# Optimization experiments

Hardware: AMD Instinct MI355X
Metric: run time of the kernel (lower is better)

Reference implementation:

```python
import jax, jax.numpy as jnp
import numpy as np

I = 2048  # input_size
O = 2048  # output_size
K = 16    # number of parallel linears

def setup_inputs() -> dict:
    key = jax.random.key(0)
    ks = jax.random.split(key, 8)
    s_in = 1.0 / np.sqrt(I)
    s_cat = 1.0 / np.sqrt(K * O)
    x = jax.random.normal(ks[0], (4, 2048, I), dtype=jnp.float32)
    W16 = jax.random.uniform(ks[1], (K, O, I), jnp.float32, -s_in, s_in)   # stacked weights of 16 Linears
    b16 = jax.random.uniform(ks[2], (K, O), jnp.float32, -s_in, s_in)
    Wf = jax.random.uniform(ks[3], (O, K * O), jnp.float32, -s_cat, s_cat)  # fusion Linear weight
    bf = jax.random.uniform(ks[4], (O,), jnp.float32, -s_cat, s_cat)
    gamma = jnp.ones((O,), jnp.float32)  # LayerNorm weight
    beta = jnp.zeros((O,), jnp.float32)  # LayerNorm bias
    return {"x": x, "W16": W16, "b16": b16, "Wf": Wf, "bf": bf, "gamma": gamma, "beta": beta}

def reference(x, W16, b16, Wf, bf, gamma, beta):
    B, S, _ = x.shape
    # 16 parallel Linears as one batched GEMM; k index order == torch.cat order
    y = jnp.einsum('bsi,koi->bsko', x, W16) + b16          # [B,S,16,O]
    combined = y.reshape(B, S, K * O)                       # concat along last dim
    fused = jnp.einsum('bsc,oc->bso', combined, Wf) + bf    # fusion linear [B,S,O]
    # LayerNorm (eps=1e-5, torch default)
    mu = jnp.mean(fused, axis=-1, keepdims=True)
    var = jnp.mean(jnp.square(fused - mu), axis=-1, keepdims=True)
    normed = (fused - mu) * jax.lax.rsqrt(var + 1e-5) * gamma + beta
    # exact (erf) GELU matching torch nn.GELU default; dropout(p=0.005) is identity at eval
    return jax.nn.gelu(normed, approximate=False)
```

## Files before the change

### kernel.cpp

```cpp
#include <hip/hip_runtime.h>
#include <hip/hip_bf16.h>
#include <math.h>


typedef __bf16 bf16_t;
typedef __bf16 bf16x8 __attribute__((ext_vector_type(8)));
typedef __bf16 bf16x4 __attribute__((ext_vector_type(4)));
typedef float  f32x4  __attribute__((ext_vector_type(4)));

#define KC 32768
#define OD 2048
#define ID 2048
#define BSROWS 8192

#define GLL16(g, l) __builtin_amdgcn_global_load_lds( \
    (const __attribute__((address_space(1))) void*)(g), \
    (__attribute__((address_space(3))) void*)(l), 16, 0, 0)

__device__ __forceinline__ float wave_sum(float v) {
#pragma unroll
  for (int o = 32; o > 0; o >>= 1) v += __shfl_down(v, o, 64);
  return v;
}

__global__ __launch_bounds__(512, 1) void gemm256(
    const bf16_t* __restrict__ A, const bf16_t* __restrict__ B,
    float* __restrict__ C, int M, int N, int lda, int ldb,
    int Ks, int nbn, int mn)
{
  __shared__ char lds[131072];
  const int tid  = threadIdx.x;
  const int lane = tid & 63;
  const int wave = tid >> 6;

  const int nwg = gridDim.x;
  const int per = nwg >> 3;
  const int swz = (blockIdx.x & 7) * per + (blockIdx.x >> 3);
  const int z   = swz / mn;
  const int rem = swz - z * mn;
  const int bm  = (rem / nbn) * 256;
  const int bn  = (rem % nbn) * 256;
  const int k0  = z * Ks;
  float* Cz = C + (size_t)z * ((size_t)M * (size_t)N);

  const int wr = wave >> 2, wc = wave & 3;
  const int frow  = lane & 15;
  const int bhalf = wc >> 1;

  const int rdsl0 = (((lane >> 4))     ^ (lane & 7)) * 16;
  const int rdsl1 = (((lane >> 4) + 4) ^ (lane & 7)) * 16;

  const int abase = wr * 16384 + frow * 128;
  const int bloc  = ((wc & 1) * 64 + frow) * 128;

  const int srow8 = tid >> 3;
  const int sw8   = (tid & 7) ^ (srow8 & 7);
  const bf16_t* gA0 = A + (size_t)(bm + srow8) * lda + k0 + sw8 * 8;
  const bf16_t* gB0 = B + (size_t)(bn + srow8) * ldb + k0 + sw8 * 8;
  const int ldw = wave * 1024;

  f32x4 acc[8][4] = {};
  bf16x8 aqE[2][2], aqO[2][2], bA[4][2], bB[4][2];
  const int NT = Ks >> 6;

#define STAGE_A_HALF(t, hf) do {                                          \
    _Pragma("unroll") for (int s_ = 0; s_ < 2; ++s_)                      \
      GLL16(gA0 + (size_t)((hf) * 128 + s_ * 64) * lda + (size_t)(t) * 64,\
            lds + (((t) & 1) << 15) + (hf) * 16384 + s_ * 8192 + ldw);    \
  } while (0)

#define STAGE_B_HALF(t, hh) do {                                          \
    _Pragma("unroll") for (int s_ = 0; s_ < 2; ++s_)                      \
      GLL16(gB0 + (size_t)((hh) * 128 + s_ * 64) * ldb + (size_t)(t) * 64,\
            lds + 65536 + ((((t) * 2 + (hh)) & 3) << 14) + s_ * 8192 + ldw); \
  } while (0)

#define READ_AQ(t, q, aq) do {                                            \
    const char* p_ = lds + (((t) & 1) << 15) + abase + (q) * 4096;        \
    aq[0][0] = *reinterpret_cast<const bf16x8*>(p_ + rdsl0);              \
    aq[0][1] = *reinterpret_cast<const bf16x8*>(p_ + rdsl1);              \
    aq[1][0] = *reinterpret_cast<const bf16x8*>(p_ + 2048 + rdsl0);       \
    aq[1][1] = *reinterpret_cast<const bf16x8*>(p_ + 2048 + rdsl1);       \
  } while (0)

#define READ_BH(t, kh, bg) do {                                           \
    const char* p_ = lds + 65536 + ((((t) * 2 + bhalf) & 3) << 14) + bloc;\
    _Pragma("unroll") for (int n_ = 0; n_ < 4; ++n_)                      \
      bg[n_][kh] = *reinterpret_cast<const bf16x8*>(                      \
          p_ + n_ * 2048 + ((kh) ? rdsl1 : rdsl0));                       \
  } while (0)

#define SYNCPH() do {                                                     \
    __builtin_amdgcn_s_barrier();                                         \
    asm volatile("s_waitcnt lgkmcnt(0)" ::: "memory");                    \
    __builtin_amdgcn_sched_barrier(0);                                    \
  } while (0)

#define MFMA_Q(q, aq, bg) do {                                            \
    __builtin_amdgcn_s_setprio(1);                                        \
    _Pragma("unroll") for (int mh_ = 0; mh_ < 2; ++mh_)                   \
      _Pragma("unroll") for (int n_ = 0; n_ < 4; ++n_) {                  \
        acc[2*(q)+mh_][n_] = __builtin_amdgcn_mfma_f32_16x16x32_bf16(     \
            aq[mh_][0], bg[n_][0], acc[2*(q)+mh_][n_], 0, 0, 0);          \
        acc[2*(q)+mh_][n_] = __builtin_amdgcn_mfma_f32_16x16x32_bf16(     \
            aq[mh_][1], bg[n_][1], acc[2*(q)+mh_][n_], 0, 0, 0);          \
      }                                                                   \
    __builtin_amdgcn_s_setprio(0);                                        \
  } while (0)

#define TILE(t, BC, BN) do {                                              \
                                                                  \
    if ((t) + 1 < NT) STAGE_A_HALF((t) + 1, 0);                           \
    READ_AQ((t), 0, aqE);                                                 \
    SYNCPH(); MFMA_Q(0, aqE, BC);                                         \
                                                                  \
    if ((t) + 1 < NT) STAGE_A_HALF((t) + 1, 1);                           \
    READ_AQ((t), 1, aqO);                                                 \
    SYNCPH(); MFMA_Q(1, aqO, BC);                                         \
    if ((t) + 1 < NT) {                \
      asm volatile("s_waitcnt vmcnt(4)" ::: "memory");                    \
      __builtin_amdgcn_s_barrier();                                       \
    }                                                                     \
                                                                  \
    if ((t) + 2 < NT) STAGE_B_HALF((t) + 2, 0);                           \
    READ_AQ((t), 2, aqE);                                                 \
    if ((t) + 1 < NT) READ_BH((t) + 1, 0, BN);                            \
    SYNCPH(); MFMA_Q(2, aqE, BC);                                         \
                                                                  \
    if ((t) + 2 < NT) STAGE_B_HALF((t) + 2, 1);                           \
    READ_AQ((t), 3, aqO);                                                 \
    if ((t) + 1 < NT) READ_BH((t) + 1, 1, BN);                            \
    SYNCPH(); MFMA_Q(3, aqO, BC);                                         \
    if ((t) + 2 < NT) {                \
      asm volatile("s_waitcnt vmcnt(4)" ::: "memory");                    \
      __builtin_amdgcn_s_barrier();                                       \
    } else if ((t) + 1 < NT) {                                            \
      asm volatile("s_waitcnt vmcnt(0)" ::: "memory");    \
      __builtin_amdgcn_s_barrier();                                       \
    }                                                                     \
  } while (0)

  STAGE_A_HALF(0, 0); STAGE_A_HALF(0, 1);
  STAGE_B_HALF(0, 0); STAGE_B_HALF(0, 1);
  STAGE_B_HALF(1, 0); STAGE_B_HALF(1, 1);
  asm volatile("s_waitcnt vmcnt(4)" ::: "memory");
  __builtin_amdgcn_s_barrier();
  READ_BH(0, 0, bA);
  READ_BH(0, 1, bA);
  asm volatile("s_waitcnt lgkmcnt(0)" ::: "memory");
  __builtin_amdgcn_sched_barrier(0);
  __builtin_amdgcn_s_barrier();

#pragma unroll 1
  for (int t = 0; t < NT; t += 2) {
    TILE(t,     bA, bB);
    TILE(t + 1, bB, bA);
  }
#undef TILE
#undef MFMA_Q
#undef SYNCPH
#undef READ_BH
#undef READ_AQ
#undef STAGE_B_HALF
#undef STAGE_A_HALF

  const int wrbase = wr * 128, wcbase = wc * 64;
  const int cr = (lane >> 4) * 4, cc = lane & 15;
#pragma unroll
  for (int m = 0; m < 8; ++m)
#pragma unroll
    for (int n = 0; n < 4; ++n) {
      size_t base = (size_t)(bm + wrbase + m * 16 + cr) * N + (bn + wcbase + n * 16 + cc);
#pragma unroll
      for (int j = 0; j < 4; ++j)
        Cz[base + (size_t)j * N] = acc[m][n][j];
    }
}

__global__ void conv_wf_beq(const float* __restrict__ Wf, const float* __restrict__ b16,
                            bf16_t* __restrict__ Wf16, float* __restrict__ beq)
{
  const int o  = blockIdx.y;
  const int cb = blockIdx.x * 2048;
  const int t  = threadIdx.x;
  const size_t gbase = (size_t)o * KC + cb + t * 8;
  const float4 v0 = *(const float4*)(Wf + gbase);
  const float4 v1 = *(const float4*)(Wf + gbase + 4);
  const float4 b0 = *(const float4*)(b16 + cb + t * 8);
  const float4 b1 = *(const float4*)(b16 + cb + t * 8 + 4);
  bf16x8 r;
  r[0] = (bf16_t)v0.x; r[1] = (bf16_t)v0.y; r[2] = (bf16_t)v0.z; r[3] = (bf16_t)v0.w;
  r[4] = (bf16_t)v1.x; r[5] = (bf16_t)v1.y; r[6] = (bf16_t)v1.z; r[7] = (bf16_t)v1.w;
  *reinterpret_cast<bf16x8*>(Wf16 + gbase) = r;
  float s = v0.x * b0.x + v0.y * b0.y + v0.z * b0.z + v0.w * b0.w
          + v1.x * b1.x + v1.y * b1.y + v1.z * b1.z + v1.w * b1.w;
  s = wave_sum(s);
  __shared__ float red[4];
  if ((t & 63) == 0) red[t >> 6] = s;
  __syncthreads();
  if (t == 0) atomicAdd(beq + o, red[0] + red[1] + red[2] + red[3]);
}

__global__ void transpose_w16(const float* __restrict__ W, bf16_t* __restrict__ T)
{
  __shared__ bf16_t tile[64][65];
  const int cb = blockIdx.x * 64;
  const int ib = blockIdx.y * 64;
  const int tx = threadIdx.x & 63;
  const int ty = threadIdx.x >> 6;
#pragma unroll
  for (int r = ty; r < 64; r += 4)
    tile[r][tx] = (bf16_t)W[(size_t)(cb + r) * ID + ib + tx];
  __syncthreads();
  const int orow = threadIdx.x >> 3;
  const int oc8  = (threadIdx.x & 7) * 8;
#pragma unroll
  for (int rr = 0; rr < 2; ++rr) {
    const int r = orow + rr * 32;
    bf16x8 v;
#pragma unroll
    for (int j = 0; j < 8; ++j) v[j] = tile[oc8 + j][r];
    *reinterpret_cast<bf16x8*>(T + (size_t)(ib + r) * KC + cb + oc8) = v;
  }
}

__global__ void conv_x(const float* __restrict__ X, bf16_t* __restrict__ X16)
{
  const size_t i = ((size_t)blockIdx.x * 256 + threadIdx.x) * 8;
  const float4 v0 = *(const float4*)(X + i);
  const float4 v1 = *(const float4*)(X + i + 4);
  bf16x8 r;
  r[0] = (bf16_t)v0.x; r[1] = (bf16_t)v0.y; r[2] = (bf16_t)v0.z; r[3] = (bf16_t)v0.w;
  r[4] = (bf16_t)v1.x; r[5] = (bf16_t)v1.y; r[6] = (bf16_t)v1.z; r[7] = (bf16_t)v1.w;
  *reinterpret_cast<bf16x8*>(X16 + i) = r;
}

__global__ void reduce_weq(const float* __restrict__ slabs, bf16_t* __restrict__ Weq)
{
  const size_t MN = (size_t)OD * ID;
  const size_t i = ((size_t)blockIdx.x * 256 + threadIdx.x) * 4;
  float4 a = *(const float4*)(slabs + i);
  float4 b = *(const float4*)(slabs + MN + i);
  float4 c = *(const float4*)(slabs + 2 * MN + i);
  float4 d = *(const float4*)(slabs + 3 * MN + i);
  bf16x4 r;
  r[0] = (bf16_t)(a.x + b.x + c.x + d.x);
  r[1] = (bf16_t)(a.y + b.y + c.y + d.y);
  r[2] = (bf16_t)(a.z + b.z + c.z + d.z);
  r[3] = (bf16_t)(a.w + b.w + c.w + d.w);
  *reinterpret_cast<bf16x4*>(Weq + i) = r;
}

__global__ __launch_bounds__(256) void ln_gelu(
    const float* __restrict__ fused, const float* __restrict__ beq,
    const float* __restrict__ bfv, const float* __restrict__ gamma,
    const float* __restrict__ beta, float* __restrict__ out)
{
  const int row = blockIdx.x;
  const int t = threadIdx.x;
  const float* fr = fused + (size_t)row * OD;
  const int c0 = t * 8;
  float v[8];
  float s = 0.f, ss = 0.f;
#pragma unroll
  for (int j = 0; j < 2; ++j) {
    float4 x  = *(const float4*)(fr  + c0 + j * 4);
    float4 bq = *(const float4*)(beq + c0 + j * 4);
    float4 bb = *(const float4*)(bfv + c0 + j * 4);
    v[j * 4 + 0] = x.x + bq.x + bb.x;
    v[j * 4 + 1] = x.y + bq.y + bb.y;
    v[j * 4 + 2] = x.z + bq.z + bb.z;
    v[j * 4 + 3] = x.w + bq.w + bb.w;
#pragma unroll
    for (int e = 0; e < 4; ++e) { float w = v[j * 4 + e]; s += w; ss += w * w; }
  }
  s = wave_sum(s); ss = wave_sum(ss);
  __shared__ float rs[4], rss[4];
  if ((t & 63) == 0) { rs[t >> 6] = s; rss[t >> 6] = ss; }
  __syncthreads();
  const float S  = rs[0] + rs[1] + rs[2] + rs[3];
  const float SS = rss[0] + rss[1] + rss[2] + rss[3];
  const float mu   = S * (1.f / OD);
  const float var  = SS * (1.f / OD) - mu * mu;
  const float rstd = rsqrtf(var + 1e-5f);
#pragma unroll
  for (int j = 0; j < 2; ++j) {
    float4 g  = *(const float4*)(gamma + c0 + j * 4);
    float4 be = *(const float4*)(beta  + c0 + j * 4);
    float4 o;
    float xn;
    xn  = (v[j * 4 + 0] - mu) * rstd * g.x + be.x; o.x = 0.5f * xn * (1.f + erff(xn * 0.70710678118f));
    xn  = (v[j * 4 + 1] - mu) * rstd * g.y + be.y; o.y = 0.5f * xn * (1.f + erff(xn * 0.70710678118f));
    xn  = (v[j * 4 + 2] - mu) * rstd * g.z + be.z; o.z = 0.5f * xn * (1.f + erff(xn * 0.70710678118f));
    xn  = (v[j * 4 + 3] - mu) * rstd * g.w + be.w; o.w = 0.5f * xn * (1.f + erff(xn * 0.70710678118f));
    *(float4*)(out + (size_t)row * OD + c0 + j * 4) = o;
  }
}

extern "C" void kernel_launch(void* const* d_in, const int* in_sizes, int n_in,
                              void* d_out, int out_size, void* d_ws, size_t ws_size,
                              hipStream_t stream) {
  const float* x     = (const float*)d_in[0];
  const float* W16   = (const float*)d_in[1];
  const float* b16   = (const float*)d_in[2];
  const float* Wf    = (const float*)d_in[3];
  const float* bfv   = (const float*)d_in[4];
  const float* gamma = (const float*)d_in[5];
  const float* beta  = (const float*)d_in[6];
  float* out = (float*)d_out;

  char* ws = (char*)d_ws;
  bf16_t* W16T  = (bf16_t*)(ws);
  bf16_t* Wf16  = (bf16_t*)(ws + 134217728);
  bf16_t* X16   = (bf16_t*)(ws + 268435456);
  bf16_t* Weq   = (bf16_t*)(ws + 301989888);
  float*  beq   = (float*)(ws + 310378496);
  float*  slabs = (float*)(ws + 310386688);
  float*  fused = slabs;

  hipMemsetAsync(beq, 0, OD * sizeof(float), stream);

  conv_wf_beq<<<dim3(16, 2048), 256, 0, stream>>>(Wf, b16, Wf16, beq);
  transpose_w16<<<dim3(KC / 64, ID / 64), 256, 0, stream>>>(W16, W16T);
  conv_x<<<(BSROWS * ID) / (256 * 8), 256, 0, stream>>>(x, X16);

  gemm256<<<256, 512, 0, stream>>>(Wf16, W16T, slabs, OD, ID, KC, KC, KC / 4, 8, 64);
  reduce_weq<<<(OD * ID) / (256 * 4), 256, 0, stream>>>(slabs, Weq);

  gemm256<<<256, 512, 0, stream>>>(X16, Weq, fused, BSROWS, OD, ID, ID, ID, 8, 256);

  ln_gelu<<<BSROWS, 256, 0, stream>>>(fused, beq, bfv, gamma, beta, out);
}
```

Baseline: 537.0 us.

## Switch GEMM inner loop to 32x32x16 MFMA with reordered A-fragment prefetch

Replaces the 16x16x32 bf16 MFMA tiling with 32x32x16 MFMAs. Each wave now holds 4x2 blocks of 32x32 accumulators, and the LDS read patterns and epilogue store mapping change to match. The A-fragment reads are also shifted one quarter ahead, so the next m-block's A data is read while the current MFMAs run, and the next tile's first block is preloaded after the barrier. The aim is fewer LDS reads per flop and better MFMA throughput, at the cost of more complex register scheduling and a different output layout that must stay correct.

```diff
diff --git a/kernel.cpp b/kernel.cpp
--- a/kernel.cpp
+++ b/kernel.cpp
@@ -7,6 +7,7 @@
 typedef __bf16 bf16x8 __attribute__((ext_vector_type(8)));
 typedef __bf16 bf16x4 __attribute__((ext_vector_type(4)));
 typedef float  f32x4  __attribute__((ext_vector_type(4)));
+typedef float  f32x16 __attribute__((ext_vector_type(16)));
 
 #define KC 32768
 #define OD 2048
@@ -44,14 +45,18 @@
   float* Cz = C + (size_t)z * ((size_t)M * (size_t)N);
 
   const int wr = wave >> 2, wc = wave & 3;
-  const int frow  = lane & 15;
   const int bhalf = wc >> 1;
-
-  const int rdsl0 = (((lane >> 4))     ^ (lane & 7)) * 16;
-  const int rdsl1 = (((lane >> 4) + 4) ^ (lane & 7)) * 16;
-
-  const int abase = wr * 16384 + frow * 128;
-  const int bloc  = ((wc & 1) * 64 + frow) * 128;
+  const int l31 = lane & 31;
+  const int lhi = lane >> 5;
+  const int lk7 = lane & 7;
+
+  const int asl0 = (((0 * 2 + lhi)) ^ lk7) * 16;
+  const int asl1 = (((1 * 2 + lhi)) ^ lk7) * 16;
+  const int asl2 = (((2 * 2 + lhi)) ^ lk7) * 16;
+  const int asl3 = (((3 * 2 + lhi)) ^ lk7) * 16;
+
+  const int abase = wr * 16384 + l31 * 128;
+  const int bloc  = ((wc & 1) * 64 + l31) * 128;
 
   const int srow8 = tid >> 3;
   const int sw8   = (tid & 7) ^ (srow8 & 7);
@@ -59,8 +64,8 @@
   const bf16_t* gB0 = B + (size_t)(bn + srow8) * ldb + k0 + sw8 * 8;
   const int ldw = wave * 1024;
 
-  f32x4 acc[8][4] = {};
-  bf16x8 aqE[2][2], aqO[2][2], bA[4][2], bB[4][2];
+  f32x16 acc[4][2] = {};
+  bf16x8 aE[4], aO[4], bA[2][4], bB[2][4];
   const int NT = Ks >> 6;
 
 #define STAGE_A_HALF(t, hf) do {                                          \
@@ -75,19 +80,20 @@
             lds + 65536 + ((((t) * 2 + (hh)) & 3) << 14) + s_ * 8192 + ldw); \
   } while (0)
 
-#define READ_AQ(t, q, aq) do {                                            \
-    const char* p_ = lds + (((t) & 1) << 15) + abase + (q) * 4096;        \
-    aq[0][0] = *reinterpret_cast<const bf16x8*>(p_ + rdsl0);              \
-    aq[0][1] = *reinterpret_cast<const bf16x8*>(p_ + rdsl1);              \
-    aq[1][0] = *reinterpret_cast<const bf16x8*>(p_ + 2048 + rdsl0);       \
-    aq[1][1] = *reinterpret_cast<const bf16x8*>(p_ + 2048 + rdsl1);       \
-  } while (0)
-
-#define READ_BH(t, kh, bg) do {                                           \
+#define READ_A32(t, mb, ar) do {                                          \
+    const char* p_ = lds + (((t) & 1) << 15) + abase + (mb) * 4096;       \
+    ar[0] = *reinterpret_cast<const bf16x8*>(p_ + asl0);                  \
+    ar[1] = *reinterpret_cast<const bf16x8*>(p_ + asl1);                  \
+    ar[2] = *reinterpret_cast<const bf16x8*>(p_ + asl2);                  \
+    ar[3] = *reinterpret_cast<const bf16x8*>(p_ + asl3);                  \
+  } while (0)
+
+#define READ_B32(t, kh, bg) do {                                          \
     const char* p_ = lds + 65536 + ((((t) * 2 + bhalf) & 3) << 14) + bloc;\
-    _Pragma("unroll") for (int n_ = 0; n_ < 4; ++n_)                      \
-      bg[n_][kh] = *reinterpret_cast<const bf16x8*>(                      \
-          p_ + n_ * 2048 + ((kh) ? rdsl1 : rdsl0));                       \
+    bg[0][(kh)*2]   = *reinterpret_cast<const bf16x8*>(p_ + ((kh) ? asl2 : asl0));          \
+    bg[0][(kh)*2+1] = *reinterpret_cast<const bf16x8*>(p_ + ((kh) ? asl3 : asl1));          \
+    bg[1][(kh)*2]   = *reinterpret_cast<const bf16x8*>(p_ + 4096 + ((kh) ? asl2 : asl0));   \
+    bg[1][(kh)*2+1] = *reinterpret_cast<const bf16x8*>(p_ + 4096 + ((kh) ? asl3 : asl1));   \
   } while (0)
 
 #define SYNCPH() do {                                                     \
@@ -96,47 +102,45 @@
     __builtin_amdgcn_sched_barrier(0);                                    \
   } while (0)
 
-#define MFMA_Q(q, aq, bg) do {                                            \
+#define MFMA_M(mb, ar, bg) do {                                           \
     __builtin_amdgcn_s_setprio(1);                                        \
-    _Pragma("unroll") for (int mh_ = 0; mh_ < 2; ++mh_)                   \
-      _Pragma("unroll") for (int n_ = 0; n_ < 4; ++n_) {                  \
-        acc[2*(q)+mh_][n_] = __builtin_amdgcn_mfma_f32_16x16x32_bf16(     \
-            aq[mh_][0], bg[n_][0], acc[2*(q)+mh_][n_], 0, 0, 0);          \
-        acc[2*(q)+mh_][n_] = __builtin_amdgcn_mfma_f32_16x16x32_bf16(     \
-            aq[mh_][1], bg[n_][1], acc[2*(q)+mh_][n_], 0, 0, 0);          \
-      }                                                                   \
+    _Pragma("unroll") for (int ks_ = 0; ks_ < 4; ++ks_)                   \
+      _Pragma("unroll") for (int nb_ = 0; nb_ < 2; ++nb_)                 \
+        acc[mb][nb_] = __builtin_amdgcn_mfma_f32_32x32x16_bf16(           \
+            ar[ks_], bg[nb_][ks_], acc[mb][nb_], 0, 0, 0);                \
     __builtin_amdgcn_s_setprio(0);                                        \
   } while (0)
 
 #define TILE(t, BC, BN) do {                                              \
                                                                   \
     if ((t) + 1 < NT) STAGE_A_HALF((t) + 1, 0);                           \
-    READ_AQ((t), 0, aqE);                                                 \
-    SYNCPH(); MFMA_Q(0, aqE, BC);                                         \
+    READ_A32((t), 1, aO);                                                 \
+    SYNCPH(); MFMA_M(0, aE, BC);                                          \
                                                                   \
     if ((t) + 1 < NT) STAGE_A_HALF((t) + 1, 1);                           \
-    READ_AQ((t), 1, aqO);                                                 \
-    SYNCPH(); MFMA_Q(1, aqO, BC);                                         \
-    if ((t) + 1 < NT) {                \
+    READ_A32((t), 2, aE);                                                 \
+    SYNCPH(); MFMA_M(1, aO, BC);                                          \
+    if ((t) + 1 < NT) {                  \
       asm volatile("s_waitcnt vmcnt(4)" ::: "memory");                    \
       __builtin_amdgcn_s_barrier();                                       \
     }                                                                     \
                                                                   \
     if ((t) + 2 < NT) STAGE_B_HALF((t) + 2, 0);                           \
-    READ_AQ((t), 2, aqE);                                                 \
-    if ((t) + 1 < NT) READ_BH((t) + 1, 0, BN);                            \
-    SYNCPH(); MFMA_Q(2, aqE, BC);                                         \
+    READ_A32((t), 3, aO);                                                 \
+    if ((t) + 1 < NT) READ_B32((t) + 1, 0, BN);                           \
+    SYNCPH(); MFMA_M(2, aE, BC);                                          \
                                                                   \
     if ((t) + 2 < NT) STAGE_B_HALF((t) + 2, 1);                           \
-    READ_AQ((t), 3, aqO);                                                 \
-    if ((t) + 1 < NT) READ_BH((t) + 1, 1, BN);                            \
-    SYNCPH(); MFMA_Q(3, aqO, BC);                                         \
-    if ((t) + 2 < NT) {                \
+    if ((t) + 1 < NT) READ_B32((t) + 1, 1, BN);                           \
+    SYNCPH(); MFMA_M(3, aO, BC);                                          \
+    if ((t) + 2 < NT) {                  \
       asm volatile("s_waitcnt vmcnt(4)" ::: "memory");                    \
       __builtin_amdgcn_s_barrier();                                       \
+      READ_A32((t) + 1, 0, aE);                      \
     } else if ((t) + 1 < NT) {                                            \
       asm volatile("s_waitcnt vmcnt(0)" ::: "memory");    \
       __builtin_amdgcn_s_barrier();                                       \
+      READ_A32((t) + 1, 0, aE);                                           \
     }                                                                     \
   } while (0)
 
@@ -145,8 +149,9 @@
   STAGE_B_HALF(1, 0); STAGE_B_HALF(1, 1);
   asm volatile("s_waitcnt vmcnt(4)" ::: "memory");
   __builtin_amdgcn_s_barrier();
-  READ_BH(0, 0, bA);
-  READ_BH(0, 1, bA);
+  READ_B32(0, 0, bA);
+  READ_B32(0, 1, bA);
+  READ_A32(0, 0, aE);
   asm volatile("s_waitcnt lgkmcnt(0)" ::: "memory");
   __builtin_amdgcn_sched_barrier(0);
   __builtin_amdgcn_s_barrier();
@@ -157,23 +162,25 @@
     TILE(t + 1, bB, bA);
   }
 #undef TILE
-#undef MFMA_Q
+#undef MFMA_M
 #undef SYNCPH
-#undef READ_BH
-#undef READ_AQ
+#undef READ_B32
+#undef READ_A32
 #undef STAGE_B_HALF
 #undef STAGE_A_HALF
 
   const int wrbase = wr * 128, wcbase = wc * 64;
-  const int cr = (lane >> 4) * 4, cc = lane & 15;
-#pragma unroll
-  for (int m = 0; m < 8; ++m)
-#pragma unroll
-    for (int n = 0; n < 4; ++n) {
-      size_t base = (size_t)(bm + wrbase + m * 16 + cr) * N + (bn + wcbase + n * 16 + cc);
-#pragma unroll
-      for (int j = 0; j < 4; ++j)
-        Cz[base + (size_t)j * N] = acc[m][n][j];
+#pragma unroll
+  for (int mb = 0; mb < 4; ++mb)
+#pragma unroll
+    for (int nb = 0; nb < 2; ++nb) {
+      const int col = bn + wcbase + nb * 32 + l31;
+      const int row0 = bm + wrbase + mb * 32 + 4 * lhi;
+#pragma unroll
+      for (int g = 0; g < 4; ++g)
+#pragma unroll
+        for (int j = 0; j < 4; ++j)
+          Cz[(size_t)(row0 + 8 * g + j) * N + col] = acc[mb][nb][g * 4 + j];
     }
 }
 
```

Result: slower. 988.8 us (+84.1%).
